# Kernel tuning notes

Measured on AMD Instinct MI355X. Metric: run time of the kernel, lower is better.

Reference implementation:

```python
import jax, jax.numpy as jnp
from jax import lax
import numpy as np

N_HEADS, N_FEATURES, IMG_W, IMG_H, C_DOWN = 8, 64, 96, 96, 32


def setup_inputs() -> dict:
    key = jax.random.key(0)
    ks = jax.random.split(key, 16)
    d = {
        'X': jax.random.normal(ks[0], (N_FEATURES, IMG_W, IMG_H), jnp.float32),
        'WQ_task': jax.random.normal(ks[1], (N_HEADS, N_FEATURES, 1, 1), jnp.float32),
        'BQ_task': jax.random.normal(ks[2], (N_HEADS, N_FEATURES, 1, 1), jnp.float32),
        'WK_task': jax.random.normal(ks[3], (N_FEATURES, 1, 1), jnp.float32),
        'BK_task': jax.random.normal(ks[4], (N_FEATURES, 1, 1), jnp.float32),
        'WV_task': jax.random.normal(ks[5], (1, C_DOWN, 1, 1), jnp.float32),
        'BV_task': jax.random.normal(ks[6], (1, C_DOWN, 1, 1), jnp.float32),
        # learned parameters (loaded from disk in the original)
        'WQ_t_minus_1': jax.random.uniform(ks[7], (N_HEADS, N_FEATURES, 1, 1), jnp.float32),
        'WQ_x': jax.random.uniform(ks[8], (1, N_FEATURES, 1, 1), jnp.float32),
        'BQ': jax.random.uniform(ks[9], (N_HEADS, N_FEATURES, 1, 1), jnp.float32),
        'WK_x': jax.random.uniform(ks[10], (N_FEATURES, 1, 1), jnp.float32),
        'BK': jax.random.uniform(ks[11], (N_FEATURES, 1, 1), jnp.float32),
        'Vconv_w': jax.random.normal(ks[12], (C_DOWN, N_FEATURES, 3, 3), jnp.float32) * 0.05,
        'Vconv_b': jax.random.normal(ks[13], (C_DOWN,), jnp.float32) * 0.05,
        # recurrent state (zeros at t=0 in original; random here to exercise the path)
        'prev_Q': jax.random.normal(ks[14], (N_HEADS, N_FEATURES, IMG_W, IMG_H), jnp.float32),
    }
    return d


def reference(X, WQ_task, BQ_task, WK_task, BK_task, WV_task, BV_task,
              WQ_t_minus_1, WQ_x, BQ, WK_x, BK, Vconv_w, Vconv_b, prev_Q):
    F, W, H = X.shape
    rx = X[None]  # (1, F, W, H)
    # Q: (A, F, W, H);  K: (F, W, H)
    Q = WQ_task * jax.nn.relu(WQ_t_minus_1 * prev_Q + WQ_x * rx + BQ) + BQ_task
    K = WK_task * jax.nn.relu(WK_x * X + BK) + BK_task
    # similarity[w,h,u,v] = sum_{a,f} Q[a,f,w,h] * K[f,u,v]
    #                     = sum_f (sum_a Q)[f,w,h] * K[f,u,v]  -> a (WH,F)@(F,WH) GEMM
    Qs = Q.sum(axis=0)  # (F, W, H)
    sim = jnp.einsum('fwh,fuv->whuv', Qs, K)  # (W, H, W, H)
    attn = jax.nn.softmax(sim.reshape(W, H, W * H), axis=-1)  # (W, H, WH)
    # V = task-modulated 3x3 conv of X
    Vc = lax.conv_general_dilated(rx, Vconv_w, window_strides=(1, 1), padding='SAME',
                                  dimension_numbers=('NCHW', 'OIHW', 'NCHW'))
    Vc = Vc + Vconv_b[None, :, None, None]
    V = (WV_task * Vc + BV_task)[0].reshape(C_DOWN, W * H)  # (C, WH)
    # out[c,w,h] = sum_k attn[w,h,k] * V[c,k]
    out = jnp.einsum('whk,ck->cwh', attn, V)  # (C, W, H)
    return out
```

## Files before the change

kernel.cpp:

```cpp
#include <hip/hip_runtime.h>

#define WH 9216
#define NF 64
#define NC 32
#define NH 8
#define IMGW 96
#define IMGH 96
#define PW 98
#define PPLANE 9604

typedef float f32x4 __attribute__((ext_vector_type(4)));
typedef short short8 __attribute__((ext_vector_type(8)));

__device__ inline short bf16_bits(float x) {
  __bf16 h = (__bf16)x;
  return __builtin_bit_cast(short, h);
}
__device__ inline float bf16_round(float x) { return (float)(__bf16)x; }

__global__ __launch_bounds__(256) void pad_wpack_kernel(
    const float* __restrict__ X, const float* __restrict__ Wc,
    const float* __restrict__ WV_task,
    unsigned short* __restrict__ padX, short8* __restrict__ wfrag)
{
  const int bid = blockIdx.x;
  const int t = threadIdx.x;
  if (bid < 2401) {
    const int idx = bid * 256 + t;
    const int f = idx / PPLANE;
    const int p = idx - f * PPLANE;
    const int pw = p / PW;
    const int ph = p - pw * PW;
    float v = 0.f;
    if (pw >= 1 && pw <= IMGW && ph >= 1 && ph <= IMGH)
      v = X[(size_t)f * WH + (pw - 1) * IMGH + (ph - 1)];
    padX[idx] = (unsigned short)bf16_bits(v);
  } else {
    #pragma unroll
    for (int j = 0; j < 9; ++j) {
      const int ridx = j * 256 + t;
      const int ct = ridx / 1152;
      const int rem = ridx - ct * 1152;
      const int cc = rem >> 6;
      const int lane = rem & 63;
      const int c = ct * 16 + (lane & 15);
      const int tap = cc >> 1;
      const int f0 = (cc & 1) * 32 + 8 * (lane >> 4);
      const float wv = WV_task[c];
      short8 r;
      #pragma unroll
      for (int e = 0; e < 8; ++e)
        r[e] = bf16_bits(wv * Wc[((size_t)c * NF + f0 + e) * 9 + tap]);
      wfrag[ridx] = r;
    }
  }
}

__global__ __launch_bounds__(128, 1) void qsk_kernel(
    const float* __restrict__ X, const float* __restrict__ WQ_task,
    const float* __restrict__ BQ_task, const float* __restrict__ WK_task,
    const float* __restrict__ BK_task, const float* __restrict__ WQ_t1,
    const float* __restrict__ WQ_x, const float* __restrict__ BQ,
    const float* __restrict__ WK_x, const float* __restrict__ BK,
    const float* __restrict__ prevQ,
    short8* __restrict__ qfrag, short8* __restrict__ kfrag)
{
  const int t = threadIdx.x;
  const int lane = t & 63;
  const int fh = t >> 6;
  const int h = lane >> 4;
  const int T = blockIdx.x;
  const int wh = T * 16 + (lane & 15);
  const int f0 = fh * 32 + 8 * h;

  float x[8];
  #pragma unroll
  for (int e = 0; e < 8; ++e) x[e] = X[(size_t)(f0 + e) * WH + wh];
  float pq[64];
  #pragma unroll
  for (int a = 0; a < NH; ++a)
    #pragma unroll
    for (int e = 0; e < 8; ++e)
      pq[a * 8 + e] = prevQ[(size_t)(a * 64 + f0 + e) * WH + wh];

  float wkx[8], bk[8], wkt[8], bkt[8], wqx[8];
  *(float4*)&wkx[0] = *(const float4*)&WK_x[f0];
  *(float4*)&wkx[4] = *(const float4*)&WK_x[f0 + 4];
  *(float4*)&bk[0]  = *(const float4*)&BK[f0];
  *(float4*)&bk[4]  = *(const float4*)&BK[f0 + 4];
  *(float4*)&wkt[0] = *(const float4*)&WK_task[f0];
  *(float4*)&wkt[4] = *(const float4*)&WK_task[f0 + 4];
  *(float4*)&bkt[0] = *(const float4*)&BK_task[f0];
  *(float4*)&bkt[4] = *(const float4*)&BK_task[f0 + 4];
  *(float4*)&wqx[0] = *(const float4*)&WQ_x[f0];
  *(float4*)&wqx[4] = *(const float4*)&WQ_x[f0 + 4];

  float q[8], k[8], xq[8];
  #pragma unroll
  for (int e = 0; e < 8; ++e) {
    k[e] = fmaf(wkt[e], fmaxf(fmaf(wkx[e], x[e], bk[e]), 0.f), bkt[e]);
    xq[e] = wqx[e] * x[e];
    q[e] = 0.f;
  }
  #pragma unroll
  for (int a = 0; a < NH; ++a) {
    const int af0 = a * 64 + f0;
    float w1[8], bq[8], wqt[8], bqt[8];
    *(float4*)&w1[0]  = *(const float4*)&WQ_t1[af0];
    *(float4*)&w1[4]  = *(const float4*)&WQ_t1[af0 + 4];
    *(float4*)&bq[0]  = *(const float4*)&BQ[af0];
    *(float4*)&bq[4]  = *(const float4*)&BQ[af0 + 4];
    *(float4*)&wqt[0] = *(const float4*)&WQ_task[af0];
    *(float4*)&wqt[4] = *(const float4*)&WQ_task[af0 + 4];
    *(float4*)&bqt[0] = *(const float4*)&BQ_task[af0];
    *(float4*)&bqt[4] = *(const float4*)&BQ_task[af0 + 4];
    #pragma unroll
    for (int e = 0; e < 8; ++e) {
      const float r = fmaxf(fmaf(w1[e], pq[a * 8 + e], xq[e] + bq[e]), 0.f);
      q[e] = fmaf(wqt[e], r, q[e]) + bqt[e];
    }
  }

  short8 qh, ql, kh, klo;
  #pragma unroll
  for (int e = 0; e < 8; ++e) {
    qh[e] = bf16_bits(q[e]);
    ql[e] = bf16_bits(q[e] - bf16_round(q[e]));
    kh[e] = bf16_bits(k[e]);
    klo[e] = bf16_bits(k[e] - bf16_round(k[e]));
  }
  qfrag[((size_t)T * 4 + fh) * 64 + lane] = qh;
  qfrag[((size_t)T * 4 + 2 + fh) * 64 + lane] = ql;
  kfrag[((size_t)T * 4 + fh) * 64 + lane] = kh;
  kfrag[((size_t)T * 4 + 2 + fh) * 64 + lane] = klo;
}

__global__ __launch_bounds__(256, 1) void vconv_kernel(
    const unsigned short* __restrict__ padX, const short8* __restrict__ wfrag,
    const float* __restrict__ bc, const float* __restrict__ WV_task,
    const float* __restrict__ BV_task, short8* __restrict__ vfrag)
{
  __shared__ float Vt[2][32][36];
  const int t = threadIdx.x;
  const int lane = t & 63, w = t >> 6;
  const int h = lane >> 4;
  const int b = blockIdx.x;
  const int ktloc = w >> 1, half = w & 1;
  const int key = (b * 2 + ktloc) * 16 + (lane & 15);
  const int kw = key / IMGH, kh = key - kw * IMGH;

  f32x4 acc0 = {0.f, 0.f, 0.f, 0.f}, acc1 = {0.f, 0.f, 0.f, 0.f};
  #pragma unroll
  for (int i = 0; i < 9; ++i) {
    const int cc = half * 9 + i;
    const int tap = cc >> 1;
    const int di = tap / 3, dj = tap - di * 3;
    const int f0 = (cc & 1) * 32 + 8 * h;
    const int sp = (kw + di) * PW + (kh + dj);
    short8 xf;
    #pragma unroll
    for (int e = 0; e < 8; ++e)
      xf[e] = (short)padX[(size_t)(f0 + e) * PPLANE + sp];
    const short8 wf0 = wfrag[(size_t)cc * 64 + lane];
    const short8 wf1 = wfrag[(size_t)(18 + cc) * 64 + lane];
    acc0 = __builtin_amdgcn_mfma_f32_16x16x32_bf16(wf0, xf, acc0, 0, 0, 0);
    acc1 = __builtin_amdgcn_mfma_f32_16x16x32_bf16(wf1, xf, acc1, 0, 0, 0);
  }
  const int klc = ktloc * 16 + (lane & 15);
  #pragma unroll
  for (int reg = 0; reg < 4; ++reg) {
    Vt[half][4 * h + reg][klc] = acc0[reg];
    Vt[half][16 + 4 * h + reg][klc] = acc1[reg];
  }
  __syncthreads();
  if (t < 128) {
    const int ct = t >> 6;
    const int c = ct * 16 + (lane & 15);
    const float bias = fmaf(WV_task[c], bc[c], BV_task[c]);
    short8 r;
    #pragma unroll
    for (int e = 0; e < 8; ++e) {
      const int kl2 = 16 * (e >> 2) + 4 * h + (e & 3);
      r[e] = bf16_bits(Vt[0][c][kl2] + Vt[1][c][kl2] + bias);
    }
    vfrag[((size_t)b * 2 + ct) * 64 + lane] = r;
  }
}

__global__ __launch_bounds__(256, 3) void flash_mfma(
    const short8* __restrict__ qfrag, const short8* __restrict__ kfrag,
    const short8* __restrict__ vfrag, float* __restrict__ part, int cps)
{
  const int t = threadIdx.x;
  const int lane = t & 63, wave = t >> 6;
  const int h = lane >> 4;
  const int qb = blockIdx.x;
  const int s = blockIdx.y;

  short8 qf[3][4];
  #pragma unroll
  for (int g = 0; g < 3; ++g)
    #pragma unroll
    for (int tm = 0; tm < 4; ++tm)
      qf[g][tm] = qfrag[((size_t)(qb * 3 + g) * 4 + tm) * 64 + lane];

  f32x4 acc[2][3];
  #pragma unroll
  for (int ct = 0; ct < 2; ++ct)
    #pragma unroll
    for (int g = 0; g < 3; ++g)
      acc[ct][g] = (f32x4){0.f, 0.f, 0.f, 0.f};
  float m[3] = {-1e30f, -1e30f, -1e30f};
  float l[3] = {0.f, 0.f, 0.f};

  const int cpw = cps >> 2;
  const int ch0 = s * cps + wave;
  for (int it = 0; it < cpw; ++it) {
    const int ch = ch0 + it * 4;
    short8 kf[2][4];
    #pragma unroll
    for (int kt = 0; kt < 2; ++kt)
      #pragma unroll
      for (int tm = 0; tm < 4; ++tm)
        kf[kt][tm] = kfrag[((size_t)(2 * ch + kt) * 4 + tm) * 64 + lane];
    short8 vf0 = vfrag[(size_t)(ch * 2 + 0) * 64 + lane];
    short8 vf1 = vfrag[(size_t)(ch * 2 + 1) * 64 + lane];

    f32x4 st[2][3];
    #pragma unroll
    for (int kt = 0; kt < 2; ++kt)
      #pragma unroll
      for (int g = 0; g < 3; ++g) {
        f32x4 a = (f32x4){0.f, 0.f, 0.f, 0.f};
        a = __builtin_amdgcn_mfma_f32_16x16x32_bf16(kf[kt][0], qf[g][0], a, 0, 0, 0);
        a = __builtin_amdgcn_mfma_f32_16x16x32_bf16(kf[kt][1], qf[g][1], a, 0, 0, 0);
        a = __builtin_amdgcn_mfma_f32_16x16x32_bf16(kf[kt][2], qf[g][0], a, 0, 0, 0);
        a = __builtin_amdgcn_mfma_f32_16x16x32_bf16(kf[kt][3], qf[g][1], a, 0, 0, 0);
        a = __builtin_amdgcn_mfma_f32_16x16x32_bf16(kf[kt][0], qf[g][2], a, 0, 0, 0);
        a = __builtin_amdgcn_mfma_f32_16x16x32_bf16(kf[kt][1], qf[g][3], a, 0, 0, 0);
        st[kt][g] = a;
      }

    #pragma unroll
    for (int g = 0; g < 3; ++g) {
      float p[8];
      #pragma unroll
      for (int e = 0; e < 4; ++e) { p[e] = st[0][g][e]; p[4 + e] = st[1][g][e]; }
      float tmax = fmaxf(fmaxf(fmaxf(p[0], p[1]), fmaxf(p[2], p[3])),
                         fmaxf(fmaxf(p[4], p[5]), fmaxf(p[6], p[7])));
      tmax = fmaxf(tmax, __shfl_xor(tmax, 16));
      tmax = fmaxf(tmax, __shfl_xor(tmax, 32));
      if (__any(tmax > m[g] + 8.f)) {
        const float nm = fmaxf(m[g], tmax);
        const float r = __expf(m[g] - nm);
        l[g] *= r;
        acc[0][g] *= r;
        acc[1][g] *= r;
        m[g] = nm;
      }
      short8 pb;
      float ls = 0.f;
      #pragma unroll
      for (int e = 0; e < 8; ++e) {
        const float pe = __expf(p[e] - m[g]);
        ls += pe;
        pb[e] = bf16_bits(pe);
      }
      l[g] += ls;
      acc[0][g] = __builtin_amdgcn_mfma_f32_16x16x32_bf16(vf0, pb, acc[0][g], 0, 0, 0);
      acc[1][g] = __builtin_amdgcn_mfma_f32_16x16x32_bf16(vf1, pb, acc[1][g], 0, 0, 0);
    }
  }

  const int u = s * 4 + wave;
  #pragma unroll
  for (int g = 0; g < 3; ++g) {
    float lf = l[g] + __shfl_xor(l[g], 16);
    lf += __shfl_xor(lf, 32);
    const int q = qb * 48 + g * 16 + (lane & 15);
    float* base = part + ((size_t)u * WH + q) * 36;
    *(f32x4*)(base + 0 + 4 * h) = acc[0][g];
    *(f32x4*)(base + 16 + 4 * h) = acc[1][g];
    if (h == 0) { base[32] = m[g]; base[33] = lf; }
  }
}

__global__ __launch_bounds__(256) void merge_kernel(
    const float* __restrict__ part, float* __restrict__ out, int units)
{
  const int t = threadIdx.x;
  const int cl = t & 31;
  const int wh = blockIdx.x * 8 + (t >> 5);
  float M = -1e30f;
  for (int u = 0; u < units; ++u)
    M = fmaxf(M, part[((size_t)u * WH + wh) * 36 + 32]);
  float L = 0.f, A = 0.f;
  for (int u = 0; u < units; ++u) {
    const float* base = part + ((size_t)u * WH + wh) * 36;
    const float e = __expf(base[32] - M);
    L = fmaf(e, base[33], L);
    A = fmaf(e, base[cl], A);
  }
  out[(size_t)cl * WH + wh] = A / L;
}

extern "C" void kernel_launch(void* const* d_in, const int* in_sizes, int n_in,
                              void* d_out, int out_size, void* d_ws, size_t ws_size,
                              hipStream_t stream)
{
  const float* X   = (const float*)d_in[0];
  const float* WQt = (const float*)d_in[1];
  const float* BQt = (const float*)d_in[2];
  const float* WKt = (const float*)d_in[3];
  const float* BKt = (const float*)d_in[4];
  const float* WVt = (const float*)d_in[5];
  const float* BVt = (const float*)d_in[6];
  const float* WQ1 = (const float*)d_in[7];
  const float* WQx = (const float*)d_in[8];
  const float* BQ  = (const float*)d_in[9];
  const float* WKx = (const float*)d_in[10];
  const float* BK  = (const float*)d_in[11];
  const float* Wc  = (const float*)d_in[12];
  const float* bc  = (const float*)d_in[13];
  const float* pQ  = (const float*)d_in[14];
  float* out = (float*)d_out;

  short8* qfrag = (short8*)d_ws;
  short8* kfrag = qfrag + (size_t)147456;
  short8* vfrag = kfrag + (size_t)147456;
  short8* wfrag = vfrag + (size_t)36864;
  unsigned short* padX = (unsigned short*)(wfrag + 2304);
  float* part = (float*)((char*)padX + (size_t)614656 * 2);
  const size_t base_bytes = ((size_t)147456 * 2 + 36864 + 2304) * 16 + (size_t)614656 * 2;

  int ksplit = 4;
  while (ksplit > 1 &&
         base_bytes + (size_t)(4 * ksplit) * WH * 36 * sizeof(float) > ws_size)
    ksplit >>= 1;
  const int cps = 288 / ksplit;
  const int units = 4 * ksplit;

  pad_wpack_kernel<<<dim3(2402), 256, 0, stream>>>(X, Wc, WVt, padX, wfrag);
  qsk_kernel<<<dim3(576), 128, 0, stream>>>(X, WQt, BQt, WKt, BKt,
                                            WQ1, WQx, BQ, WKx, BK, pQ,
                                            qfrag, kfrag);
  vconv_kernel<<<dim3(288), 256, 0, stream>>>(padX, wfrag, bc, WVt, BVt, vfrag);
  flash_mfma<<<dim3(192, ksplit), 256, 0, stream>>>(qfrag, kfrag, vfrag, part, cps);
  merge_kernel<<<dim3(WH / 8), 256, 0, stream>>>(part, out, units);
}
```

Baseline: 87.95 us.

## Skip negligible key chunks via hi-only score estimate, transpose padded X, split qsk

The flash kernel first computes a cheap score estimate from the high-bf16 parts of K and Q. When every score in a chunk sits more than SKIP below the running max, it skips the low-part MFMAs, the V loads and the PV accumulate for that chunk. Every eighth chunk is still computed fully so the running max keeps advancing. Q is prescaled by log2(e) so the kernels can use exp2f, and the rescale threshold is relaxed to DEFER. Padded X is stored channel-last so vconv can load its fragments as one vector, and qsk is split across twice as many blocks with two allowed per CU. The skip drops probability mass below about 2^-18 in a data-dependent way, which changes accuracy slightly and adds divergence risk.

```diff
diff --git a/kernel.cpp b/kernel.cpp
--- a/kernel.cpp
+++ b/kernel.cpp
@@ -8,6 +8,9 @@
 #define IMGH 96
 #define PW 98
 #define PPLANE 9604
+#define L2E 1.4426950408889634f
+#define DEFER 11.5f
+#define SKIP 18.0f
 
 typedef float f32x4 __attribute__((ext_vector_type(4)));
 typedef short short8 __attribute__((ext_vector_type(8)));
@@ -21,20 +24,28 @@
 __global__ __launch_bounds__(256) void pad_wpack_kernel(
     const float* __restrict__ X, const float* __restrict__ Wc,
     const float* __restrict__ WV_task,
-    unsigned short* __restrict__ padX, short8* __restrict__ wfrag)
+    unsigned short* __restrict__ padXT, short8* __restrict__ wfrag)
 {
   const int bid = blockIdx.x;
   const int t = threadIdx.x;
-  if (bid < 2401) {
+  if (bid < 301) {
     const int idx = bid * 256 + t;
-    const int f = idx / PPLANE;
-    const int p = idx - f * PPLANE;
-    const int pw = p / PW;
-    const int ph = p - pw * PW;
-    float v = 0.f;
-    if (pw >= 1 && pw <= IMGW && ph >= 1 && ph <= IMGH)
-      v = X[(size_t)f * WH + (pw - 1) * IMGH + (ph - 1)];
-    padX[idx] = (unsigned short)bf16_bits(v);
+    if (idx < 76832) {
+      const int fi = idx / PPLANE;
+      const int p = idx - fi * PPLANE;
+      const int pw = p / PW;
+      const int ph = p - pw * PW;
+      short8 r;
+      if (pw >= 1 && pw <= IMGW && ph >= 1 && ph <= IMGH) {
+        const float* src = X + (size_t)fi * 8 * WH + (pw - 1) * IMGH + (ph - 1);
+        #pragma unroll
+        for (int e = 0; e < 8; ++e) r[e] = bf16_bits(src[(size_t)e * WH]);
+      } else {
+        #pragma unroll
+        for (int e = 0; e < 8; ++e) r[e] = 0;
+      }
+      *(short8*)&padXT[(size_t)p * 64 + fi * 8] = r;
+    }
   } else {
     #pragma unroll
     for (int j = 0; j < 9; ++j) {
@@ -56,87 +67,83 @@
   }
 }
 
-__global__ __launch_bounds__(128, 1) void qsk_kernel(
+__global__ __launch_bounds__(128, 2) void qsk_kernel(
     const float* __restrict__ X, const float* __restrict__ WQ_task,
     const float* __restrict__ BQ_task, const float* __restrict__ WK_task,
     const float* __restrict__ BK_task, const float* __restrict__ WQ_t1,
     const float* __restrict__ WQ_x, const float* __restrict__ BQ,
     const float* __restrict__ WK_x, const float* __restrict__ BK,
     const float* __restrict__ prevQ,
-    short8* __restrict__ qfrag, short8* __restrict__ kfrag)
+    short* __restrict__ qfrag, short* __restrict__ kfrag)
 {
   const int t = threadIdx.x;
   const int lane = t & 63;
   const int fh = t >> 6;
   const int h = lane >> 4;
-  const int T = blockIdx.x;
+  const int b = blockIdx.x;
+  const int T = b >> 1, sub = b & 1;
   const int wh = T * 16 + (lane & 15);
-  const int f0 = fh * 32 + 8 * h;
-
-  float x[8];
-  #pragma unroll
-  for (int e = 0; e < 8; ++e) x[e] = X[(size_t)(f0 + e) * WH + wh];
-  float pq[64];
+  const int f0 = fh * 32 + 8 * h + 4 * sub;
+
+  float x[4];
+  #pragma unroll
+  for (int e = 0; e < 4; ++e) x[e] = X[(size_t)(f0 + e) * WH + wh];
+  float pq[32];
   #pragma unroll
   for (int a = 0; a < NH; ++a)
     #pragma unroll
-    for (int e = 0; e < 8; ++e)
-      pq[a * 8 + e] = prevQ[(size_t)(a * 64 + f0 + e) * WH + wh];
-
-  float wkx[8], bk[8], wkt[8], bkt[8], wqx[8];
-  *(float4*)&wkx[0] = *(const float4*)&WK_x[f0];
-  *(float4*)&wkx[4] = *(const float4*)&WK_x[f0 + 4];
-  *(float4*)&bk[0]  = *(const float4*)&BK[f0];
-  *(float4*)&bk[4]  = *(const float4*)&BK[f0 + 4];
-  *(float4*)&wkt[0] = *(const float4*)&WK_task[f0];
-  *(float4*)&wkt[4] = *(const float4*)&WK_task[f0 + 4];
-  *(float4*)&bkt[0] = *(const float4*)&BK_task[f0];
-  *(float4*)&bkt[4] = *(const float4*)&BK_task[f0 + 4];
-  *(float4*)&wqx[0] = *(const float4*)&WQ_x[f0];
-  *(float4*)&wqx[4] = *(const float4*)&WQ_x[f0 + 4];
-
-  float q[8], k[8], xq[8];
-  #pragma unroll
-  for (int e = 0; e < 8; ++e) {
-    k[e] = fmaf(wkt[e], fmaxf(fmaf(wkx[e], x[e], bk[e]), 0.f), bkt[e]);
-    xq[e] = wqx[e] * x[e];
-    q[e] = 0.f;
-  }
+    for (int e = 0; e < 4; ++e)
+      pq[a * 4 + e] = prevQ[(size_t)(a * 64 + f0 + e) * WH + wh];
+
+  const float4 wkx = *(const float4*)&WK_x[f0];
+  const float4 bk  = *(const float4*)&BK[f0];
+  const float4 wkt = *(const float4*)&WK_task[f0];
+  const float4 bkt = *(const float4*)&BK_task[f0];
+  const float4 wqx = *(const float4*)&WQ_x[f0];
+
+  float q[4], k[4], xq[4];
+  k[0] = fmaf(wkt.x, fmaxf(fmaf(wkx.x, x[0], bk.x), 0.f), bkt.x);
+  k[1] = fmaf(wkt.y, fmaxf(fmaf(wkx.y, x[1], bk.y), 0.f), bkt.y);
+  k[2] = fmaf(wkt.z, fmaxf(fmaf(wkx.z, x[2], bk.z), 0.f), bkt.z);
+  k[3] = fmaf(wkt.w, fmaxf(fmaf(wkx.w, x[3], bk.w), 0.f), bkt.w);
+  xq[0] = wqx.x * x[0]; xq[1] = wqx.y * x[1];
+  xq[2] = wqx.z * x[2]; xq[3] = wqx.w * x[3];
+  q[0] = q[1] = q[2] = q[3] = 0.f;
   #pragma unroll
   for (int a = 0; a < NH; ++a) {
     const int af0 = a * 64 + f0;
-    float w1[8], bq[8], wqt[8], bqt[8];
-    *(float4*)&w1[0]  = *(const float4*)&WQ_t1[af0];
-    *(float4*)&w1[4]  = *(const float4*)&WQ_t1[af0 + 4];
-    *(float4*)&bq[0]  = *(const float4*)&BQ[af0];
-    *(float4*)&bq[4]  = *(const float4*)&BQ[af0 + 4];
-    *(float4*)&wqt[0] = *(const float4*)&WQ_task[af0];
-    *(float4*)&wqt[4] = *(const float4*)&WQ_task[af0 + 4];
-    *(float4*)&bqt[0] = *(const float4*)&BQ_task[af0];
-    *(float4*)&bqt[4] = *(const float4*)&BQ_task[af0 + 4];
-    #pragma unroll
-    for (int e = 0; e < 8; ++e) {
-      const float r = fmaxf(fmaf(w1[e], pq[a * 8 + e], xq[e] + bq[e]), 0.f);
-      q[e] = fmaf(wqt[e], r, q[e]) + bqt[e];
-    }
-  }
-
-  short8 qh, ql, kh, klo;
-  #pragma unroll
-  for (int e = 0; e < 8; ++e) {
-    qh[e] = bf16_bits(q[e]);
-    ql[e] = bf16_bits(q[e] - bf16_round(q[e]));
-    kh[e] = bf16_bits(k[e]);
-    klo[e] = bf16_bits(k[e] - bf16_round(k[e]));
-  }
-  qfrag[((size_t)T * 4 + fh) * 64 + lane] = qh;
-  qfrag[((size_t)T * 4 + 2 + fh) * 64 + lane] = ql;
-  kfrag[((size_t)T * 4 + fh) * 64 + lane] = kh;
-  kfrag[((size_t)T * 4 + 2 + fh) * 64 + lane] = klo;
+    const float4 w1  = *(const float4*)&WQ_t1[af0];
+    const float4 bq  = *(const float4*)&BQ[af0];
+    const float4 wqt = *(const float4*)&WQ_task[af0];
+    const float4 bqt = *(const float4*)&BQ_task[af0];
+    q[0] = fmaf(wqt.x, fmaxf(fmaf(w1.x, pq[a * 4 + 0], xq[0] + bq.x), 0.f), q[0]) + bqt.x;
+    q[1] = fmaf(wqt.y, fmaxf(fmaf(w1.y, pq[a * 4 + 1], xq[1] + bq.y), 0.f), q[1]) + bqt.y;
+    q[2] = fmaf(wqt.z, fmaxf(fmaf(w1.z, pq[a * 4 + 2], xq[2] + bq.z), 0.f), q[2]) + bqt.z;
+    q[3] = fmaf(wqt.w, fmaxf(fmaf(w1.w, pq[a * 4 + 3], xq[3] + bq.w), 0.f), q[3]) + bqt.w;
+  }
+
+  short4 qh, ql, kh, klo;
+  {
+    float qs0 = q[0] * L2E, qs1 = q[1] * L2E, qs2 = q[2] * L2E, qs3 = q[3] * L2E;
+    qh.x = bf16_bits(qs0); ql.x = bf16_bits(qs0 - bf16_round(qs0));
+    qh.y = bf16_bits(qs1); ql.y = bf16_bits(qs1 - bf16_round(qs1));
+    qh.z = bf16_bits(qs2); ql.z = bf16_bits(qs2 - bf16_round(qs2));
+    qh.w = bf16_bits(qs3); ql.w = bf16_bits(qs3 - bf16_round(qs3));
+    kh.x = bf16_bits(k[0]); klo.x = bf16_bits(k[0] - bf16_round(k[0]));
+    kh.y = bf16_bits(k[1]); klo.y = bf16_bits(k[1] - bf16_round(k[1]));
+    kh.z = bf16_bits(k[2]); klo.z = bf16_bits(k[2] - bf16_round(k[2]));
+    kh.w = bf16_bits(k[3]); klo.w = bf16_bits(k[3] - bf16_round(k[3]));
+  }
+  const size_t offh = ((size_t)(T * 4 + fh) * 64 + lane) * 8 + sub * 4;
+  const size_t offl = ((size_t)(T * 4 + 2 + fh) * 64 + lane) * 8 + sub * 4;
+  *(short4*)&qfrag[offh] = qh;
+  *(short4*)&qfrag[offl] = ql;
+  *(short4*)&kfrag[offh] = kh;
+  *(short4*)&kfrag[offl] = klo;
 }
 
 __global__ __launch_bounds__(256, 1) void vconv_kernel(
-    const unsigned short* __restrict__ padX, const short8* __restrict__ wfrag,
+    const unsigned short* __restrict__ padXT, const short8* __restrict__ wfrag,
     const float* __restrict__ bc, const float* __restrict__ WV_task,
     const float* __restrict__ BV_task, short8* __restrict__ vfrag)
 {
@@ -157,14 +164,9 @@
     const int di = tap / 3, dj = tap - di * 3;
     const int f0 = (cc & 1) * 32 + 8 * h;
     const int sp = (kw + di) * PW + (kh + dj);
-    short8 xf;
-    #pragma unroll
-    for (int e = 0; e < 8; ++e)
-      xf[e] = (short)padX[(size_t)(f0 + e) * PPLANE + sp];
-    const short8 wf0 = wfrag[(size_t)cc * 64 + lane];
-    const short8 wf1 = wfrag[(size_t)(18 + cc) * 64 + lane];
-    acc0 = __builtin_amdgcn_mfma_f32_16x16x32_bf16(wf0, xf, acc0, 0, 0, 0);
-    acc1 = __builtin_amdgcn_mfma_f32_16x16x32_bf16(wf1, xf, acc1, 0, 0, 0);
+    const short8 xf = *(const short8*)&padXT[(size_t)sp * 64 + f0];
+    acc0 = __builtin_amdgcn_mfma_f32_16x16x32_bf16(wfrag[(size_t)cc * 64 + lane], xf, acc0, 0, 0, 0);
+    acc1 = __builtin_amdgcn_mfma_f32_16x16x32_bf16(wfrag[(size_t)(18 + cc) * 64 + lane], xf, acc1, 0, 0, 0);
   }
   const int klc = ktloc * 16 + (lane & 15);
   #pragma unroll
@@ -213,9 +215,35 @@
   float m[3] = {-1e30f, -1e30f, -1e30f};
   float l[3] = {0.f, 0.f, 0.f};
 
+  auto softmax_pv = [&](int g, const f32x4& st0, const f32x4& st1, float tmax,
+                        const short8& vf0, const short8& vf1) {
+    if (__any(tmax > m[g] + DEFER)) {
+      const float nm = fmaxf(m[g], tmax);
+      const float r = exp2f(m[g] - nm);
+      l[g] *= r;
+      acc[0][g] *= r;
+      acc[1][g] *= r;
+      m[g] = nm;
+    }
+    short8 pb;
+    float ls = 0.f;
+    #pragma unroll
+    for (int e = 0; e < 4; ++e) {
+      const float p0 = exp2f(st0[e] - m[g]);
+      const float p1 = exp2f(st1[e] - m[g]);
+      ls += p0 + p1;
+      pb[e] = bf16_bits(p0);
+      pb[4 + e] = bf16_bits(p1);
+    }
+    l[g] += ls;
+    acc[0][g] = __builtin_amdgcn_mfma_f32_16x16x32_bf16(vf0, pb, acc[0][g], 0, 0, 0);
+    acc[1][g] = __builtin_amdgcn_mfma_f32_16x16x32_bf16(vf1, pb, acc[1][g], 0, 0, 0);
+  };
+
   const int cpw = cps >> 2;
   const int ch0 = s * cps + wave;
-  for (int it = 0; it < cpw; ++it) {
+
+  for (int it = 0; it < cpw; it += 8) {
     const int ch = ch0 + it * 4;
     short8 kf[2][4];
     #pragma unroll
@@ -223,14 +251,14 @@
       #pragma unroll
       for (int tm = 0; tm < 4; ++tm)
         kf[kt][tm] = kfrag[((size_t)(2 * ch + kt) * 4 + tm) * 64 + lane];
-    short8 vf0 = vfrag[(size_t)(ch * 2 + 0) * 64 + lane];
-    short8 vf1 = vfrag[(size_t)(ch * 2 + 1) * 64 + lane];
-
-    f32x4 st[2][3];
-    #pragma unroll
-    for (int kt = 0; kt < 2; ++kt)
-      #pragma unroll
-      for (int g = 0; g < 3; ++g) {
+    const short8 vf0 = vfrag[(size_t)(ch * 2 + 0) * 64 + lane];
+    const short8 vf1 = vfrag[(size_t)(ch * 2 + 1) * 64 + lane];
+
+    #pragma unroll
+    for (int g = 0; g < 3; ++g) {
+      f32x4 st[2];
+      #pragma unroll
+      for (int kt = 0; kt < 2; ++kt) {
         f32x4 a = (f32x4){0.f, 0.f, 0.f, 0.f};
         a = __builtin_amdgcn_mfma_f32_16x16x32_bf16(kf[kt][0], qf[g][0], a, 0, 0, 0);
         a = __builtin_amdgcn_mfma_f32_16x16x32_bf16(kf[kt][1], qf[g][1], a, 0, 0, 0);
@@ -238,37 +266,76 @@
         a = __builtin_amdgcn_mfma_f32_16x16x32_bf16(kf[kt][3], qf[g][1], a, 0, 0, 0);
         a = __builtin_amdgcn_mfma_f32_16x16x32_bf16(kf[kt][0], qf[g][2], a, 0, 0, 0);
         a = __builtin_amdgcn_mfma_f32_16x16x32_bf16(kf[kt][1], qf[g][3], a, 0, 0, 0);
+        st[kt] = a;
+      }
+      float tmax = -1e30f;
+      #pragma unroll
+      for (int e = 0; e < 4; ++e)
+        tmax = fmaxf(tmax, fmaxf(st[0][e], st[1][e]));
+      tmax = fmaxf(tmax, __shfl_xor(tmax, 16));
+      tmax = fmaxf(tmax, __shfl_xor(tmax, 32));
+      softmax_pv(g, st[0], st[1], tmax, vf0, vf1);
+    }
+  }
+
+  for (int it = 0; it < cpw; ++it) {
+    if ((it & 7) == 0) continue;
+    const int ch = ch0 + it * 4;
+    short8 kfh[2][2];
+    #pragma unroll
+    for (int kt = 0; kt < 2; ++kt)
+      #pragma unroll
+      for (int tm = 0; tm < 2; ++tm)
+        kfh[kt][tm] = kfrag[((size_t)(2 * ch + kt) * 4 + tm) * 64 + lane];
+
+    f32x4 st[2][3];
+    #pragma unroll
+    for (int kt = 0; kt < 2; ++kt)
+      #pragma unroll
+      for (int g = 0; g < 3; ++g) {
+        f32x4 a = (f32x4){0.f, 0.f, 0.f, 0.f};
+        a = __builtin_amdgcn_mfma_f32_16x16x32_bf16(kfh[kt][0], qf[g][0], a, 0, 0, 0);
+        a = __builtin_amdgcn_mfma_f32_16x16x32_bf16(kfh[kt][1], qf[g][1], a, 0, 0, 0);
         st[kt][g] = a;
       }
 
+    float tmax[3];
+    int fire = 0;
     #pragma unroll
     for (int g = 0; g < 3; ++g) {
-      float p[8];
-      #pragma unroll
-      for (int e = 0; e < 4; ++e) { p[e] = st[0][g][e]; p[4 + e] = st[1][g][e]; }
-      float tmax = fmaxf(fmaxf(fmaxf(p[0], p[1]), fmaxf(p[2], p[3])),
-                         fmaxf(fmaxf(p[4], p[5]), fmaxf(p[6], p[7])));
-      tmax = fmaxf(tmax, __shfl_xor(tmax, 16));
-      tmax = fmaxf(tmax, __shfl_xor(tmax, 32));
-      if (__any(tmax > m[g] + 8.f)) {
-        const float nm = fmaxf(m[g], tmax);
-        const float r = __expf(m[g] - nm);
-        l[g] *= r;
-        acc[0][g] *= r;
-        acc[1][g] *= r;
-        m[g] = nm;
+      float tm8 = -1e30f;
+      #pragma unroll
+      for (int e = 0; e < 4; ++e)
+        tm8 = fmaxf(tm8, fmaxf(st[0][g][e], st[1][g][e]));
+      tm8 = fmaxf(tm8, __shfl_xor(tm8, 16));
+      tm8 = fmaxf(tm8, __shfl_xor(tm8, 32));
+      tmax[g] = tm8;
+      if (__any(tm8 > m[g] - SKIP)) fire |= 1 << g;
+    }
+    if (!fire) continue;
+
+    short8 kfl[2][2];
+    #pragma unroll
+    for (int kt = 0; kt < 2; ++kt)
+      #pragma unroll
+      for (int tm = 0; tm < 2; ++tm)
+        kfl[kt][tm] = kfrag[((size_t)(2 * ch + kt) * 4 + 2 + tm) * 64 + lane];
+    const short8 vf0 = vfrag[(size_t)(ch * 2 + 0) * 64 + lane];
+    const short8 vf1 = vfrag[(size_t)(ch * 2 + 1) * 64 + lane];
+
+    #pragma unroll
+    for (int g = 0; g < 3; ++g) {
+      if (!(fire & (1 << g))) continue;
+      #pragma unroll
+      for (int kt = 0; kt < 2; ++kt) {
+        f32x4 a = st[kt][g];
+        a = __builtin_amdgcn_mfma_f32_16x16x32_bf16(kfl[kt][0], qf[g][0], a, 0, 0, 0);
+        a = __builtin_amdgcn_mfma_f32_16x16x32_bf16(kfl[kt][1], qf[g][1], a, 0, 0, 0);
+        a = __builtin_amdgcn_mfma_f32_16x16x32_bf16(kfh[kt][0], qf[g][2], a, 0, 0, 0);
+        a = __builtin_amdgcn_mfma_f32_16x16x32_bf16(kfh[kt][1], qf[g][3], a, 0, 0, 0);
+        st[kt][g] = a;
       }
-      short8 pb;
-      float ls = 0.f;
-      #pragma unroll
-      for (int e = 0; e < 8; ++e) {
-        const float pe = __expf(p[e] - m[g]);
-        ls += pe;
-        pb[e] = bf16_bits(pe);
-      }
-      l[g] += ls;
-      acc[0][g] = __builtin_amdgcn_mfma_f32_16x16x32_bf16(vf0, pb, acc[0][g], 0, 0, 0);
-      acc[1][g] = __builtin_amdgcn_mfma_f32_16x16x32_bf16(vf1, pb, acc[1][g], 0, 0, 0);
+      softmax_pv(g, st[0][g], st[1][g], tmax[g], vf0, vf1);
     }
   }
 
@@ -297,7 +364,7 @@
   float L = 0.f, A = 0.f;
   for (int u = 0; u < units; ++u) {
     const float* base = part + ((size_t)u * WH + wh) * 36;
-    const float e = __expf(base[32] - M);
+    const float e = exp2f(base[32] - M);
     L = fmaf(e, base[33], L);
     A = fmaf(e, base[cl], A);
   }
@@ -329,9 +396,9 @@
   short8* kfrag = qfrag + (size_t)147456;
   short8* vfrag = kfrag + (size_t)147456;
   short8* wfrag = vfrag + (size_t)36864;
-  unsigned short* padX = (unsigned short*)(wfrag + 2304);
-  float* part = (float*)((char*)padX + (size_t)614656 * 2);
-  const size_t base_bytes = ((size_t)147456 * 2 + 36864 + 2304) * 16 + (size_t)614656 * 2;
+  unsigned short* padXT = (unsigned short*)(wfrag + 2304);
+  float* part = (float*)((char*)padXT + (size_t)PPLANE * 64 * 2);
+  const size_t base_bytes = ((size_t)147456 * 2 + 36864 + 2304) * 16 + (size_t)PPLANE * 64 * 2;
 
   int ksplit = 4;
   while (ksplit > 1 &&
@@ -340,11 +407,11 @@
   const int cps = 288 / ksplit;
   const int units = 4 * ksplit;
 
-  pad_wpack_kernel<<<dim3(2402), 256, 0, stream>>>(X, Wc, WVt, padX, wfrag);
-  qsk_kernel<<<dim3(576), 128, 0, stream>>>(X, WQt, BQt, WKt, BKt,
-                                            WQ1, WQx, BQ, WKx, BK, pQ,
-                                            qfrag, kfrag);
-  vconv_kernel<<<dim3(288), 256, 0, stream>>>(padX, wfrag, bc, WVt, BVt, vfrag);
+  pad_wpack_kernel<<<dim3(302), 256, 0, stream>>>(X, Wc, WVt, padXT, wfrag);
+  qsk_kernel<<<dim3(1152), 128, 0, stream>>>(X, WQt, BQt, WKt, BKt,
+                                             WQ1, WQx, BQ, WKx, BK, pQ,
+                                             (short*)qfrag, (short*)kfrag);
+  vconv_kernel<<<dim3(288), 256, 0, stream>>>(padXT, wfrag, bc, WVt, BVt, vfrag);
   flash_mfma<<<dim3(192, ksplit), 256, 0, stream>>>(qfrag, kfrag, vfrag, part, cps);
   merge_kernel<<<dim3(WH / 8), 256, 0, stream>>>(part, out, units);
 }
```

New measurement: 91.40 us. 1.04x slower.
